# Kernel optimization log

Measured on AMD Instinct MI355X. Metric: run time of the kernel, lower is better.

Reference implementation:

```python
import jax, jax.numpy as jnp
import numpy as np

B, N, K, D, C = 2, 8192, 16, 64, 3


def setup_inputs() -> dict:
    key = jax.random.key(0)
    ks = jax.random.split(key, 12)
    s = 0.05
    return {
        "xyz": jax.random.normal(ks[0], (B, N, C), jnp.float32),
        "feats": jax.random.normal(ks[1], (B, N, D), jnp.float32),
        "w_qs": jax.random.normal(ks[2], (D, D), jnp.float32) * s,
        "w_ks": jax.random.normal(ks[3], (D, D), jnp.float32) * s,
        "w_vs": jax.random.normal(ks[4], (D, D), jnp.float32) * s,
        "delta_w1": jax.random.normal(ks[5], (C, D), jnp.float32) * s,
        "delta_b1": jnp.zeros((D,), jnp.float32),
        "delta_w2": jax.random.normal(ks[6], (D, D), jnp.float32) * s,
        "delta_b2": jnp.zeros((D,), jnp.float32),
        "gamma_w1": jax.random.normal(ks[7], (D, D), jnp.float32) * s,
        "gamma_b1": jnp.zeros((D,), jnp.float32),
        "gamma_w2": jax.random.normal(ks[8], (D, D), jnp.float32) * s,
        "gamma_b2": jnp.zeros((D,), jnp.float32),
        "bn_gamma": jnp.ones((D,), jnp.float32),
        "bn_beta": jnp.zeros((D,), jnp.float32),
        "k": K,
    }


def _mlp(x, w1, b1, w2, b2):
    return jax.nn.relu(x @ w1 + b1) @ w2 + b2


def _gather(points, idx):
    # points [B,N,C], idx [B,N,K] -> [B,N,K,C]
    return jax.vmap(lambda p, i: p[i])(points, idx)


def reference(xyz, feats, w_qs, w_ks, w_vs, delta_w1, delta_b1, delta_w2, delta_b2,
              gamma_w1, gamma_b1, gamma_w2, gamma_b2, bn_gamma, bn_beta, k):
    # KNN via squared pairwise distances (expansion form, avoids [B,N,N,3] temp)
    sq = jnp.sum(xyz * xyz, axis=-1)  # [B,N]
    dists = sq[:, :, None] + sq[:, None, :] - 2.0 * jnp.einsum('bnc,bmc->bnm', xyz, xyz)
    _, knn_idx = jax.lax.top_k(-dists, k)  # ascending distance, [B,N,K]

    knn_xyz = _gather(xyz, knn_idx)                 # [B,N,K,3]
    q = feats @ w_qs                                # [B,N,D]
    k_attn = _gather(feats @ w_ks, knn_idx)         # [B,N,K,D]
    v_attn = _gather(feats @ w_vs, knn_idx)         # [B,N,K,D]

    pos = _mlp(xyz[:, :, None] - knn_xyz, delta_w1, delta_b1, delta_w2, delta_b2)  # [B,N,K,D]
    attn = _mlp(q[:, :, None] - k_attn + pos, gamma_w1, gamma_b1, gamma_w2, gamma_b2)
    attn = jax.nn.softmax(attn, axis=-2)            # softmax over neighbors

    res = jnp.einsum('bnkf,bnkf->bnf', attn, v_attn + pos)
    res = res + feats

    # BatchNorm1d (training mode): normalize per channel over (B, N)
    mean = jnp.mean(res, axis=(0, 1))
    var = jnp.var(res, axis=(0, 1))
    res = (res - mean) * jax.lax.rsqrt(var + 1e-5) * bn_gamma + bn_beta
    return res
```

## Files before the change

kernel.cpp:

```cpp
#include <hip/hip_runtime.h>
#include <hip/hip_bf16.h>

#define BN 16384
#define NPTS 8192
#define KNN 16

typedef __attribute__((ext_vector_type(8))) short bf16x8;
typedef __attribute__((ext_vector_type(4))) float f32x4;
typedef __attribute__((ext_vector_type(4))) unsigned short u16x4;

static __device__ __forceinline__ unsigned short f2bf(float f) {
    union { float f; unsigned u; } v; v.f = f;
    unsigned r = v.u + 0x7fffu + ((v.u >> 16) & 1u);
    return (unsigned short)(r >> 16);
}

__global__ __launch_bounds__(256) void pack_xyz(const float* __restrict__ xyz,
                                                float4* __restrict__ xyz4) {
    int i = blockIdx.x * 256 + threadIdx.x;
    if (i < BN) {
        float x = xyz[i * 3 + 0], y = xyz[i * 3 + 1], z = xyz[i * 3 + 2];
        xyz4[i] = make_float4(x, y, z, x * x + y * y + z * z);
    }
}

__global__ __launch_bounds__(256) void knn_kernel(const float4* __restrict__ xyz4,
                                                  int* __restrict__ knn_idx) {
    __shared__ float sred[4];
    __shared__ int scnt[4];
    __shared__ float ck[256];
    __shared__ int ci[256];
    __shared__ int scounter;
    int row = blockIdx.x;
    int b = row >> 13, n = row & (NPTS - 1);
    const float4* base = xyz4 + b * NPTS;
    int tid = threadIdx.x;
    int lane = tid & 63, wid = tid >> 6;
    float4 p = base[n];

    float dreg[32];
    float lmin = 1e30f;
#pragma unroll
    for (int i = 0; i < 32; i++) {
        int j = tid + (i << 8);
        float4 c = base[j];
        float dot = fmaf(p.x, c.x, fmaf(p.y, c.y, p.z * c.z));
        float d = p.w + c.w - 2.f * dot;
        dreg[i] = d;
        lmin = fminf(lmin, d);
    }

    float wmax = lmin;
#pragma unroll
    for (int off = 32; off; off >>= 1) wmax = fmaxf(wmax, __shfl_xor(wmax, off, 64));
    if (lane == 0) sred[wid] = wmax;
    if (tid == 0) scounter = 0;
    __syncthreads();
    float hi = fmaxf(fmaxf(sred[0], sred[1]), fmaxf(sred[2], sred[3])) * 1.0001f + 1e-6f;
    float lo = 0.f;
    float T = hi;

    for (int iter = 0; iter < 24; iter++) {
        float mid = 0.5f * (lo + hi);
        int cnt = 0;
#pragma unroll
        for (int i = 0; i < 32; i++) cnt += (dreg[i] < mid) ? 1 : 0;
#pragma unroll
        for (int off = 32; off; off >>= 1) cnt += __shfl_xor(cnt, off, 64);
        __syncthreads();
        if (lane == 0) scnt[wid] = cnt;
        __syncthreads();
        int total = scnt[0] + scnt[1] + scnt[2] + scnt[3];
        if (total >= 16 && total <= 128) { T = mid; break; }
        if (total < 16) lo = mid; else hi = mid;
        T = hi;
    }
    __syncthreads();

#pragma unroll
    for (int i = 0; i < 32; i++) {
        if (dreg[i] < T) {
            int pos = atomicAdd(&scounter, 1);
            if (pos < 256) { ck[pos] = dreg[i]; ci[pos] = tid + (i << 8); }
        }
    }
    __syncthreads();
    int cc = min(scounter, 256);

    if (tid < cc) {
        float myk = ck[tid]; int myi = ci[tid];
        int rank = 0;
        for (int j2 = 0; j2 < cc; j2++) {
            float kj = ck[j2]; int ij = ci[j2];
            rank += (kj < myk || (kj == myk && ij < myi)) ? 1 : 0;
        }
        if (rank < 16) knn_idx[row * 16 + rank] = myi;
    }
}

__global__ __launch_bounds__(256) void qkv_kernel(const float* __restrict__ feats,
                                                  const float* __restrict__ wq,
                                                  const float* __restrict__ wk,
                                                  const float* __restrict__ wv,
                                                  float* __restrict__ Q,
                                                  float* __restrict__ Kf,
                                                  float* __restrict__ Vf) {
    __shared__ float swq[4096], swk[4096], swv[4096], fr[256];
    int tid = threadIdx.x;
    for (int i = tid; i < 1024; i += 256) {
        ((float4*)swq)[i] = ((const float4*)wq)[i];
        ((float4*)swk)[i] = ((const float4*)wk)[i];
        ((float4*)swv)[i] = ((const float4*)wv)[i];
    }
    int row0 = blockIdx.x * 64;
    int c = tid & 63, rl = tid >> 6;
    for (int rg = 0; rg < 16; rg++) {
        __syncthreads();
        fr[tid] = feats[(row0 + rg * 4) * 64 + tid];
        __syncthreads();
        float aq = 0.f, ak = 0.f, av = 0.f;
        int fb = rl * 64;
        for (int kk = 0; kk < 64; kk++) {
            float f = fr[fb + kk];
            aq = fmaf(f, swq[kk * 64 + c], aq);
            ak = fmaf(f, swk[kk * 64 + c], ak);
            av = fmaf(f, swv[kk * 64 + c], av);
        }
        int row = row0 + rg * 4 + rl;
        Q[row * 64 + c] = aq;
        Kf[row * 64 + c] = ak;
        Vf[row * 64 + c] = av;
    }
}

__global__ __launch_bounds__(256, 2) void attn_mfma(
    const float4* __restrict__ xyz4, const int* __restrict__ knn_idx,
    const float* __restrict__ Q, const float* __restrict__ Kf, const float* __restrict__ Vf,
    const float* __restrict__ feats,
    const float* __restrict__ dw1, const float* __restrict__ db1,
    const float* __restrict__ dw2, const float* __restrict__ db2,
    const float* __restrict__ gw1, const float* __restrict__ gb1,
    const float* __restrict__ gw2,
    float* __restrict__ res) {
    __shared__ __align__(16) unsigned short sWd2[64 * 68];
    __shared__ __align__(16) unsigned short sWg1[64 * 68];
    __shared__ __align__(16) unsigned short sWg2[64 * 68];
    __shared__ __align__(16) unsigned short sA[256 * 72];
    __shared__ int sidx[256];
    __shared__ float sdw1[256];

    int tid = threadIdx.x;
    int w = tid >> 6, lane = tid & 63, quad = lane >> 4, col = lane & 15;
    int r0 = blockIdx.x * 16;

    for (int i = tid; i < 4096; i += 256) {
        int e = i >> 6, c = i & 63;
        sWd2[c * 68 + e] = f2bf(dw2[i]);
        sWg1[c * 68 + e] = f2bf(gw1[i]);
        sWg2[c * 68 + e] = f2bf(gw2[i]);
    }
    if (tid < 192) sdw1[tid] = dw1[tid];
    else sdw1[tid] = db1[tid - 192];
    {
        int brow = r0 + (tid >> 4);
        int b = brow >> 13;
        sidx[tid] = b * NPTS + knn_idx[brow * 16 + (tid & 15)];
    }
    __syncthreads();

    {
        int m = tid;
        int brow = r0 + (m >> 4);
        float4 p = xyz4[brow];
        float4 nb = xyz4[sidx[m]];
        float rx = p.x - nb.x, ry = p.y - nb.y, rz = p.z - nb.z;
        for (int c0 = 0; c0 < 64; c0 += 8) {
            bf16x8 v;
#pragma unroll
            for (int cc = 0; cc < 8; cc++) {
                int c = c0 + cc;
                float h = sdw1[192 + c] + rx * sdw1[c] + ry * sdw1[64 + c] + rz * sdw1[128 + c];
                v[cc] = (short)f2bf(fmaxf(h, 0.f));
            }
            *(bf16x8*)&sA[m * 72 + c0] = v;
        }
    }

    int m0 = w * 64;
    bf16x8 af[4][2];

#pragma unroll
    for (int mt = 0; mt < 4; mt++)
#pragma unroll
        for (int k2 = 0; k2 < 2; k2++)
            af[mt][k2] = *(const bf16x8*)&sA[(m0 + mt * 16 + col) * 72 + quad * 8 + k2 * 32];

    f32x4 pos[4][4];
#pragma unroll
    for (int nt = 0; nt < 4; nt++) {
        float bias = db2[nt * 16 + col];
        bf16x8 b0, b1;
        {
            const unsigned short* p0 = &sWd2[(nt * 16 + col) * 68 + quad * 8];
            u16x4 l0 = *(const u16x4*)p0, h0 = *(const u16x4*)(p0 + 4);
            u16x4 l1 = *(const u16x4*)(p0 + 32), h1 = *(const u16x4*)(p0 + 36);
#pragma unroll
            for (int z = 0; z < 4; z++) { b0[z] = (short)l0[z]; b0[z+4] = (short)h0[z]; b1[z] = (short)l1[z]; b1[z+4] = (short)h1[z]; }
        }
#pragma unroll
        for (int mt = 0; mt < 4; mt++) {
            f32x4 acc = {bias, bias, bias, bias};
            acc = __builtin_amdgcn_mfma_f32_16x16x32_bf16(af[mt][0], b0, acc, 0, 0, 0);
            acc = __builtin_amdgcn_mfma_f32_16x16x32_bf16(af[mt][1], b1, acc, 0, 0, 0);
            pos[mt][nt] = acc;
        }
    }

#pragma unroll
    for (int mt = 0; mt < 4; mt++) {
        int row = r0 + w * 4 + mt;
        int gx[4];
#pragma unroll
        for (int r = 0; r < 4; r++) gx[r] = sidx[w * 64 + mt * 16 + quad * 4 + r];
#pragma unroll
        for (int nt = 0; nt < 4; nt++) {
            int c = nt * 16 + col;
            float qv = Q[row * 64 + c];
#pragma unroll
            for (int r = 0; r < 4; r++) {
                float tv = qv - Kf[gx[r] * 64 + c] + pos[mt][nt][r];
                sA[(m0 + mt * 16 + quad * 4 + r) * 72 + c] = f2bf(tv);
            }
        }
    }

#pragma unroll
    for (int mt = 0; mt < 4; mt++)
#pragma unroll
        for (int k2 = 0; k2 < 2; k2++)
            af[mt][k2] = *(const bf16x8*)&sA[(m0 + mt * 16 + col) * 72 + quad * 8 + k2 * 32];

    f32x4 cc4[4][4];
#pragma unroll
    for (int nt = 0; nt < 4; nt++) {
        float bias = gb1[nt * 16 + col];
        bf16x8 b0, b1;
        {
            const unsigned short* p0 = &sWg1[(nt * 16 + col) * 68 + quad * 8];
            u16x4 l0 = *(const u16x4*)p0, h0 = *(const u16x4*)(p0 + 4);
            u16x4 l1 = *(const u16x4*)(p0 + 32), h1 = *(const u16x4*)(p0 + 36);
#pragma unroll
            for (int z = 0; z < 4; z++) { b0[z] = (short)l0[z]; b0[z+4] = (short)h0[z]; b1[z] = (short)l1[z]; b1[z+4] = (short)h1[z]; }
        }
#pragma unroll
        for (int mt = 0; mt < 4; mt++) {
            f32x4 acc = {bias, bias, bias, bias};
            acc = __builtin_amdgcn_mfma_f32_16x16x32_bf16(af[mt][0], b0, acc, 0, 0, 0);
            acc = __builtin_amdgcn_mfma_f32_16x16x32_bf16(af[mt][1], b1, acc, 0, 0, 0);
            cc4[mt][nt] = acc;
        }
    }
#pragma unroll
    for (int mt = 0; mt < 4; mt++)
#pragma unroll
        for (int nt = 0; nt < 4; nt++)
#pragma unroll
            for (int r = 0; r < 4; r++)
                sA[(m0 + mt * 16 + quad * 4 + r) * 72 + nt * 16 + col] = f2bf(fmaxf(cc4[mt][nt][r], 0.f));

#pragma unroll
    for (int mt = 0; mt < 4; mt++)
#pragma unroll
        for (int k2 = 0; k2 < 2; k2++)
            af[mt][k2] = *(const bf16x8*)&sA[(m0 + mt * 16 + col) * 72 + quad * 8 + k2 * 32];

#pragma unroll
    for (int nt = 0; nt < 4; nt++) {
        bf16x8 b0, b1;
        {
            const unsigned short* p0 = &sWg2[(nt * 16 + col) * 68 + quad * 8];
            u16x4 l0 = *(const u16x4*)p0, h0 = *(const u16x4*)(p0 + 4);
            u16x4 l1 = *(const u16x4*)(p0 + 32), h1 = *(const u16x4*)(p0 + 36);
#pragma unroll
            for (int z = 0; z < 4; z++) { b0[z] = (short)l0[z]; b0[z+4] = (short)h0[z]; b1[z] = (short)l1[z]; b1[z+4] = (short)h1[z]; }
        }
#pragma unroll
        for (int mt = 0; mt < 4; mt++) {
            f32x4 acc = {0.f, 0.f, 0.f, 0.f};
            acc = __builtin_amdgcn_mfma_f32_16x16x32_bf16(af[mt][0], b0, acc, 0, 0, 0);
            acc = __builtin_amdgcn_mfma_f32_16x16x32_bf16(af[mt][1], b1, acc, 0, 0, 0);
            cc4[mt][nt] = acc;
        }
    }

#pragma unroll
    for (int mt = 0; mt < 4; mt++) {
        int row = r0 + w * 4 + mt;
        int gx[4];
#pragma unroll
        for (int r = 0; r < 4; r++) gx[r] = sidx[w * 64 + mt * 16 + quad * 4 + r];
#pragma unroll
        for (int nt = 0; nt < 4; nt++) {
            int c = nt * 16 + col;
            f32x4 a = cc4[mt][nt];
            float mx = fmaxf(fmaxf(a[0], a[1]), fmaxf(a[2], a[3]));
            mx = fmaxf(mx, __shfl_xor(mx, 16, 64));
            mx = fmaxf(mx, __shfl_xor(mx, 32, 64));
            float es = 0.f, ws = 0.f;
#pragma unroll
            for (int r = 0; r < 4; r++) {
                float e = __expf(a[r] - mx);
                float vv = Vf[gx[r] * 64 + c] + pos[mt][nt][r];
                es += e;
                ws = fmaf(e, vv, ws);
            }
            es += __shfl_xor(es, 16, 64); es += __shfl_xor(es, 32, 64);
            ws += __shfl_xor(ws, 16, 64); ws += __shfl_xor(ws, 32, 64);
            if (quad == 0) {
                res[row * 64 + c] = ws / es + feats[row * 64 + c];
            }
        }
    }
}

__global__ __launch_bounds__(256) void reduce_kernel(const float* __restrict__ res,
                                                     float* __restrict__ accum) {
    __shared__ float sa[256], sq[256];
    int tid = threadIdx.x;
    const float* basep = res + blockIdx.x * 4096;
    float s = 0.f, q = 0.f;
#pragma unroll
    for (int i = 0; i < 16; i++) {
        float v = basep[i * 256 + tid];
        s += v;
        q = fmaf(v, v, q);
    }
    sa[tid] = s; sq[tid] = q;
    __syncthreads();
    if (tid < 64) {
        float ss = sa[tid] + sa[tid + 64] + sa[tid + 128] + sa[tid + 192];
        float qq = sq[tid] + sq[tid + 64] + sq[tid + 128] + sq[tid + 192];
        atomicAdd(&accum[tid], ss);
        atomicAdd(&accum[64 + tid], qq);
    }
}

__global__ __launch_bounds__(256) void norm_kernel(const float* __restrict__ res,
                                                   const float* __restrict__ accum,
                                                   const float* __restrict__ bng,
                                                   const float* __restrict__ bnb,
                                                   float* __restrict__ out) {
    int i = blockIdx.x * 256 + threadIdx.x;
    int c = i & 63;
    float mean = accum[c] * (1.f / 16384.f);
    float var = accum[64 + c] * (1.f / 16384.f) - mean * mean;
    float sc = rsqrtf(var + 1e-5f) * bng[c];
    out[i] = fmaf(res[i] - mean, sc, bnb[c]);
}

extern "C" void kernel_launch(void* const* d_in, const int* in_sizes, int n_in,
                              void* d_out, int out_size, void* d_ws, size_t ws_size,
                              hipStream_t stream) {
    const float* xyz  = (const float*)d_in[0];
    const float* feats = (const float*)d_in[1];
    const float* w_qs = (const float*)d_in[2];
    const float* w_ks = (const float*)d_in[3];
    const float* w_vs = (const float*)d_in[4];
    const float* dw1 = (const float*)d_in[5];
    const float* db1 = (const float*)d_in[6];
    const float* dw2 = (const float*)d_in[7];
    const float* db2 = (const float*)d_in[8];
    const float* gw1 = (const float*)d_in[9];
    const float* gb1 = (const float*)d_in[10];
    const float* gw2 = (const float*)d_in[11];
    const float* bng = (const float*)d_in[13];
    const float* bnb = (const float*)d_in[14];

    char* ws = (char*)d_ws;
    float4* xyz4 = (float4*)ws;
    int* knn    = (int*)(ws + 262144);
    float* Q    = (float*)(ws + 1310720);
    float* Kf   = (float*)(ws + 5505024);
    float* Vf   = (float*)(ws + 9699328);
    float* res  = (float*)(ws + 13893632);
    float* accum = (float*)(ws + 18087936);

    hipMemsetAsync(accum, 0, 512, stream);
    pack_xyz<<<64, 256, 0, stream>>>(xyz, xyz4);
    knn_kernel<<<16384, 256, 0, stream>>>(xyz4, knn);
    qkv_kernel<<<256, 256, 0, stream>>>(feats, w_qs, w_ks, w_vs, Q, Kf, Vf);
    attn_mfma<<<1024, 256, 0, stream>>>(xyz4, knn, Q, Kf, Vf, feats,
                                        dw1, db1, dw2, db2, gw1, gb1, gw2, res);
    reduce_kernel<<<256, 256, 0, stream>>>(res, accum);
    norm_kernel<<<4096, 256, 0, stream>>>(res, accum, bng, bnb, (float*)d_out);
}
```

Measured before the change: 284.0 us.

## Batch 16 KNN queries per block and replace bisection with a group-min threshold

The KNN kernel now handles 16 query points per block instead of one. Each candidate point load from global memory is reused across all 16 queries. The 24-step bisection search for a distance threshold, with its two block barriers per step, is replaced by one pass. That pass takes the minimum distance within each group of 16 lanes and sets the threshold to the maximum of those 16 group minima, which guarantees at least 16 candidates. Distances are recomputed in a second pass, not held in registers. The trade-offs are more register pressure, 32 KB of shared memory for candidate lists, and a risk that a candidate list overflows its 256-entry cap when many points fall under the looser threshold.

Measured after the change: 308.5 us. +8.6%, slower.

```diff
diff --git a/kernel.cpp b/kernel.cpp
--- a/kernel.cpp
+++ b/kernel.cpp
@@ -24,77 +24,84 @@
     }
 }
 
-__global__ __launch_bounds__(256) void knn_kernel(const float4* __restrict__ xyz4,
-                                                  int* __restrict__ knn_idx) {
-    __shared__ float sred[4];
-    __shared__ int scnt[4];
-    __shared__ float ck[256];
-    __shared__ int ci[256];
-    __shared__ int scounter;
-    int row = blockIdx.x;
-    int b = row >> 13, n = row & (NPTS - 1);
-    const float4* base = xyz4 + b * NPTS;
-    int tid = threadIdx.x;
-    int lane = tid & 63, wid = tid >> 6;
-    float4 p = base[n];
-
-    float dreg[32];
-    float lmin = 1e30f;
-#pragma unroll
+__global__ __launch_bounds__(256, 2) void knn_kernel(const float4* __restrict__ xyz4,
+                                                     int* __restrict__ knn_idx) {
+    __shared__ float wmaxs[4][16];
+    __shared__ int   cnt[16];
+    __shared__ float ckey[16 * 256];
+    __shared__ int   cidx[16 * 256];
+    int tid = threadIdx.x, lane = tid & 63, w = tid >> 6;
+    int r0 = blockIdx.x * 16;
+    int b = r0 >> 13;
+    const float4* __restrict__ base = xyz4 + b * NPTS;
+
+    float qx[16], qy[16], qz[16], qw[16];
+#pragma unroll
+    for (int rr = 0; rr < 16; rr++) {
+        float4 q = xyz4[r0 + rr];
+        qx[rr] = q.x; qy[rr] = q.y; qz[rr] = q.z; qw[rr] = q.w;
+    }
+    if (tid < 16) cnt[tid] = 0;
+
+    float minv[16];
+#pragma unroll
+    for (int rr = 0; rr < 16; rr++) minv[rr] = 3e38f;
+
+#pragma unroll 4
     for (int i = 0; i < 32; i++) {
-        int j = tid + (i << 8);
-        float4 c = base[j];
-        float dot = fmaf(p.x, c.x, fmaf(p.y, c.y, p.z * c.z));
-        float d = p.w + c.w - 2.f * dot;
-        dreg[i] = d;
-        lmin = fminf(lmin, d);
-    }
-
-    float wmax = lmin;
-#pragma unroll
-    for (int off = 32; off; off >>= 1) wmax = fmaxf(wmax, __shfl_xor(wmax, off, 64));
-    if (lane == 0) sred[wid] = wmax;
-    if (tid == 0) scounter = 0;
+        float4 c = base[tid + (i << 8)];
+#pragma unroll
+        for (int rr = 0; rr < 16; rr++) {
+            float dot = fmaf(qx[rr], c.x, fmaf(qy[rr], c.y, qz[rr] * c.z));
+            float d = fmaf(-2.f, dot, qw[rr] + c.w);
+            minv[rr] = fminf(minv[rr], d);
+        }
+    }
+
+#pragma unroll
+    for (int rr = 0; rr < 16; rr++) {
+        float v = minv[rr];
+        v = fminf(v, __shfl_xor(v, 1, 64));
+        v = fminf(v, __shfl_xor(v, 2, 64));
+        v = fminf(v, __shfl_xor(v, 4, 64));
+        v = fminf(v, __shfl_xor(v, 8, 64));
+        v = fmaxf(v, __shfl_xor(v, 16, 64));
+        v = fmaxf(v, __shfl_xor(v, 32, 64));
+        if (lane == 0) wmaxs[w][rr] = v;
+    }
     __syncthreads();
-    float hi = fmaxf(fmaxf(sred[0], sred[1]), fmaxf(sred[2], sred[3])) * 1.0001f + 1e-6f;
-    float lo = 0.f;
-    float T = hi;
-
-    for (int iter = 0; iter < 24; iter++) {
-        float mid = 0.5f * (lo + hi);
-        int cnt = 0;
-#pragma unroll
-        for (int i = 0; i < 32; i++) cnt += (dreg[i] < mid) ? 1 : 0;
-#pragma unroll
-        for (int off = 32; off; off >>= 1) cnt += __shfl_xor(cnt, off, 64);
-        __syncthreads();
-        if (lane == 0) scnt[wid] = cnt;
-        __syncthreads();
-        int total = scnt[0] + scnt[1] + scnt[2] + scnt[3];
-        if (total >= 16 && total <= 128) { T = mid; break; }
-        if (total < 16) lo = mid; else hi = mid;
-        T = hi;
+    float T[16];
+#pragma unroll
+    for (int rr = 0; rr < 16; rr++)
+        T[rr] = fmaxf(fmaxf(wmaxs[0][rr], wmaxs[1][rr]),
+                      fmaxf(wmaxs[2][rr], wmaxs[3][rr]));
+
+#pragma unroll 4
+    for (int i = 0; i < 32; i++) {
+        float4 c = base[tid + (i << 8)];
+#pragma unroll
+        for (int rr = 0; rr < 16; rr++) {
+            float dot = fmaf(qx[rr], c.x, fmaf(qy[rr], c.y, qz[rr] * c.z));
+            float d = fmaf(-2.f, dot, qw[rr] + c.w);
+            if (d <= T[rr]) {
+                int p = atomicAdd(&cnt[rr], 1);
+                if (p < 256) { ckey[rr * 256 + p] = d; cidx[rr * 256 + p] = tid + (i << 8); }
+            }
+        }
     }
     __syncthreads();
 
-#pragma unroll
-    for (int i = 0; i < 32; i++) {
-        if (dreg[i] < T) {
-            int pos = atomicAdd(&scounter, 1);
-            if (pos < 256) { ck[pos] = dreg[i]; ci[pos] = tid + (i << 8); }
-        }
-    }
-    __syncthreads();
-    int cc = min(scounter, 256);
-
-    if (tid < cc) {
-        float myk = ck[tid]; int myi = ci[tid];
-        int rank = 0;
-        for (int j2 = 0; j2 < cc; j2++) {
-            float kj = ck[j2]; int ij = ci[j2];
-            rank += (kj < myk || (kj == myk && ij < myi)) ? 1 : 0;
-        }
-        if (rank < 16) knn_idx[row * 16 + rank] = myi;
+    for (int rr = w; rr < 16; rr += 4) {
+        int cc = min(cnt[rr], 256);
+        for (int s = lane; s < cc; s += 64) {
+            float myk = ckey[rr * 256 + s]; int myi = cidx[rr * 256 + s];
+            int rank = 0;
+            for (int j2 = 0; j2 < cc; j2++) {
+                float kj = ckey[rr * 256 + j2]; int ij = cidx[rr * 256 + j2];
+                rank += (kj < myk || (kj == myk && ij < myi)) ? 1 : 0;
+            }
+            if (rank < 16) knn_idx[(r0 + rr) * 16 + rank] = myi;
+        }
     }
 }
 
@@ -387,7 +394,7 @@
 
     hipMemsetAsync(accum, 0, 512, stream);
     pack_xyz<<<64, 256, 0, stream>>>(xyz, xyz4);
-    knn_kernel<<<16384, 256, 0, stream>>>(xyz4, knn);
+    knn_kernel<<<1024, 256, 0, stream>>>(xyz4, knn);
     qkv_kernel<<<256, 256, 0, stream>>>(feats, w_qs, w_ks, w_vs, Q, Kf, Vf);
     attn_mfma<<<1024, 256, 0, stream>>>(xyz4, knn, Q, Kf, Vf, feats,
                                         dw1, db1, dw2, db2, gw1, gb1, gw2, res);
```
